# Kernel optimization log

Measured on AMD Instinct MI355X. Metric: run time of the kernel, lower is better.

The kernel has to match this reference:

```python
import jax, jax.numpy as jnp
import numpy as np

B, S, D, L = 2, 1024, 1024, 8
HQ, HK, DH = 16, 4, 64          # query heads, kv heads, head_dim = D // HQ
FF, V = 2816, 32000             # FFN hidden (2/3*4D rounded to 256), vocab
EPS = 1e-5
THETA = 500000.0


def setup_inputs() -> dict:
    key = jax.random.key(0)
    ks = jax.random.split(key, 12)
    s = 0.02
    n = lambda k, sh: jax.random.normal(k, sh, dtype=jnp.float32) * s
    return {
        "tokens": jax.random.randint(ks[0], (B, S), 0, V),
        "start_pos": 0,
        "tok_emb": n(ks[1], (V, D)),
        "wq": n(ks[2], (L, D, HQ * DH)),
        "wk": n(ks[3], (L, D, HK * DH)),
        "wv": n(ks[4], (L, D, HK * DH)),
        "wo": n(ks[5], (L, HQ * DH, D)),
        "w1": n(ks[6], (L, D, FF)),
        "w2": n(ks[7], (L, FF, D)),
        "w3": n(ks[8], (L, D, FF)),
        "attn_norm_w": jnp.ones((L, D), jnp.float32),
        "ffn_norm_w": jnp.ones((L, D), jnp.float32),
        "final_norm_w": jnp.ones((D,), jnp.float32),
        "out_w": n(ks[9], (D, V)),
    }


def _rope_cos_sin(start, seqlen):
    freqs = 1.0 / (THETA ** (jnp.arange(0, DH, 2, dtype=jnp.float32) / DH))  # [DH/2]
    t = jnp.arange(start, start + seqlen, dtype=jnp.float32)
    ang = jnp.outer(t, freqs)  # [S, DH/2]
    return jnp.cos(ang), jnp.sin(ang)


def _apply_rope(x, cos, sin):
    # x: [B,S,H,DH]; pairs (even, odd) rotated by complex freqs_cis, as in apply_rotary_emb
    xr = x.reshape(x.shape[:-1] + (DH // 2, 2))
    a, b = xr[..., 0], xr[..., 1]
    c = cos[None, :, None, :]
    s = sin[None, :, None, :]
    out = jnp.stack([a * c - b * s, a * s + b * c], axis=-1)
    return out.reshape(x.shape)


def _rmsnorm(x, w):
    return x * jax.lax.rsqrt(jnp.mean(x * x, axis=-1, keepdims=True) + EPS) * w


def reference(tokens, start_pos, tok_emb, wq, wk, wv, wo, w1, w2, w3,
              attn_norm_w, ffn_norm_w, final_norm_w, out_w):
    h = tok_emb[tokens]  # [B,S,D]
    cos, sin = _rope_cos_sin(start_pos, S)
    # strictly-upper-triangular -inf causal mask (seqlen > 1 branch)
    idx = jnp.arange(S)
    mask = jnp.where(idx[None, :] > idx[:, None], -jnp.inf, 0.0).astype(h.dtype)

    def block(h, p):
        wq_, wk_, wv_, wo_, w1_, w2_, w3_, anw, fnw = p
        x = _rmsnorm(h, anw)
        q = (x @ wq_).reshape(B, S, HQ, DH)
        k = (x @ wk_).reshape(B, S, HK, DH)
        v = (x @ wv_).reshape(B, S, HK, DH)
        q = _apply_rope(q, cos, sin)
        k = _apply_rope(k, cos, sin)
        # start_pos=0: cache slice [:, :seqlen] == freshly written k/v; GQA repeat_kv
        k = jnp.repeat(k, HQ // HK, axis=2)  # [B,S,HQ,DH]
        v = jnp.repeat(v, HQ // HK, axis=2)
        scores = jnp.einsum('bqhd,bkhd->bhqk', q, k) / (DH ** 0.5) + mask
        attn = jax.nn.softmax(scores.astype(jnp.float32), axis=-1).astype(q.dtype)
        o = jnp.einsum('bhqk,bkhd->bqhd', attn, v).reshape(B, S, HQ * DH)
        h = h + o @ wo_
        x2 = _rmsnorm(h, fnw)
        ff = (jax.nn.silu(x2 @ w1_) * (x2 @ w3_)) @ w2_
        return h + ff, None

    h, _ = jax.lax.scan(block, h, (wq, wk, wv, wo, w1, w2, w3, attn_norm_w, ffn_norm_w))
    return (_rmsnorm(h, final_norm_w) @ out_w).astype(jnp.float32)
```

## Files before the change

kernel.cpp:

```cpp
#include <hip/hip_runtime.h>
#include <hip/hip_bf16.h>

typedef __bf16 bf16;
typedef __bf16 bf16x8 __attribute__((ext_vector_type(8)));
typedef float f32x4 __attribute__((ext_vector_type(4)));

#define B_ 2
#define S_ 1024
#define D_ 1024
#define L_ 8
#define HQ_ 16
#define HK_ 4
#define DH_ 64
#define FF_ 2816
#define V_ 32000

#define LGKM0 { asm volatile("s_waitcnt lgkmcnt(0)" ::: "memory"); __builtin_amdgcn_sched_barrier(0); }

__global__ __launch_bounds__(256) void embed_k(const int* __restrict__ toks,
                                               const float* __restrict__ emb,
                                               float* __restrict__ h) {
  int row = blockIdx.x;
  int tok = toks[row];
  f32x4 v = *(const f32x4*)&emb[(size_t)tok * D_ + threadIdx.x * 4];
  *(f32x4*)&h[(size_t)row * D_ + threadIdx.x * 4] = v;
}

__global__ __launch_bounds__(256) void ropetab_k(float* __restrict__ tab) {
  int i = blockIdx.x * 256 + threadIdx.x;
  if (i >= S_ * 32) return;
  int d = i & 31, s = i >> 5;
  float f = expf(-(2.0f * d / 64.0f) * logf(500000.0f));
  float ang = (float)s * f;
  tab[i * 2]     = cosf(ang);
  tab[i * 2 + 1] = sinf(ang);
}

__global__ __launch_bounds__(256) void rmsnorm_k(const float* __restrict__ x,
                                                 const float* __restrict__ w,
                                                 bf16* __restrict__ out) {
  int row = blockIdx.x;
  const float* xr = x + (size_t)row * D_;
  int base = threadIdx.x * 4;
  f32x4 v = *(const f32x4*)&xr[base];
  float ss = v[0]*v[0] + v[1]*v[1] + v[2]*v[2] + v[3]*v[3];
  for (int m = 1; m < 64; m <<= 1) ss += __shfl_xor(ss, m, 64);
  __shared__ float partial[4];
  if ((threadIdx.x & 63) == 0) partial[threadIdx.x >> 6] = ss;
  __syncthreads();
  float tot = partial[0] + partial[1] + partial[2] + partial[3];
  float rr = rsqrtf(tot * (1.0f / D_) + 1e-5f);
  f32x4 wv = *(const f32x4*)&w[base];
  bf16* o = out + (size_t)row * D_ + base;
  o[0] = (bf16)(v[0] * rr * wv[0]);
  o[1] = (bf16)(v[1] * rr * wv[1]);
  o[2] = (bf16)(v[2] * rr * wv[2]);
  o[3] = (bf16)(v[3] * rr * wv[3]);
}

__global__ __launch_bounds__(256) void redrms_k(const float* __restrict__ p,
                                                float* __restrict__ h,
                                                const float* __restrict__ w,
                                                bf16* __restrict__ out) {
  int row = blockIdx.x;
  int base = threadIdx.x * 4;
  size_t ix = (size_t)row * D_ + base;
  f32x4 a = *(const f32x4*)&p[ix];
  f32x4 bb = *(const f32x4*)&p[ix + 2097152];
  f32x4 v = *(const f32x4*)&h[ix];
  v += a + bb;
  *(f32x4*)&h[ix] = v;
  float ss = v[0]*v[0] + v[1]*v[1] + v[2]*v[2] + v[3]*v[3];
  for (int m = 1; m < 64; m <<= 1) ss += __shfl_xor(ss, m, 64);
  __shared__ float partial[4];
  if ((threadIdx.x & 63) == 0) partial[threadIdx.x >> 6] = ss;
  __syncthreads();
  float tot = partial[0] + partial[1] + partial[2] + partial[3];
  float rr = rsqrtf(tot * (1.0f / D_) + 1e-5f);
  f32x4 wv = *(const f32x4*)&w[base];
  bf16* o = out + (size_t)row * D_ + base;
  o[0] = (bf16)(v[0] * rr * wv[0]);
  o[1] = (bf16)(v[1] * rr * wv[1]);
  o[2] = (bf16)(v[2] * rr * wv[2]);
  o[3] = (bf16)(v[3] * rr * wv[3]);
}

__global__ __launch_bounds__(256) void transpose_cvt(const float* __restrict__ src,
                                                     bf16* __restrict__ dst,
                                                     int K, int N,
                                                     long long srcStride, long long dstStride,
                                                     int rowMul, int rowAdd) {
  __shared__ float tile[32][33];
  int bx = blockIdx.x, by = blockIdx.y, z = blockIdx.z;
  src += (size_t)z * srcStride;
  dst += (size_t)z * dstStride;
  int tx = threadIdx.x & 31, ty = threadIdx.x >> 5;
#pragma unroll
  for (int i = 0; i < 4; ++i) {
    int r = ty + i * 8;
    tile[r][tx] = src[(size_t)(by * 32 + r) * N + bx * 32 + tx];
  }
  __syncthreads();
#pragma unroll
  for (int i = 0; i < 4; ++i) {
    int r = ty + i * 8;
    dst[(size_t)((bx * 32 + r) * rowMul + rowAdd) * K + by * 32 + tx] = (bf16)tile[tx][r];
  }
}

template <int EPI, int BM>
__global__ __launch_bounds__(256) void gemm_bt(const bf16* __restrict__ A,
                                               const bf16* __restrict__ BT,
                                               void* __restrict__ Cout,
                                               const float* __restrict__ R,
                                               int M, int N, int K,
                                               int lda, int ldb,
                                               int zKoff, long long partStride) {
  constexpr int MR = BM / 32;
  __shared__ bf16 As[BM * 64];
  __shared__ bf16 Bs[128 * 64];
  const int t = threadIdx.x;
  const int w = t >> 6, l = t & 63;
  const int l15 = l & 15, l4 = l >> 4;
  const int bm = blockIdx.x * BM, bn = blockIdx.y * 128;
  const int wr = w >> 1, wc = w & 1;
  const int z = blockIdx.z;

  const bf16* Az = A + (size_t)z * zKoff;
  const bf16* Bz = BT + (size_t)z * zKoff;
  float* Cz = (float*)Cout + (size_t)z * partStride;

  const int srow = t >> 3, scol = (t & 7) * 8;
  const bf16* ag = &Az[(size_t)(bm + srow) * lda + scol];
  const bf16* bg = &Bz[(size_t)(bn + srow) * ldb + scol];
  const int ldsbase = (t & 192) * 8;

  f32x4 acc[MR][4] = {};

  for (int k0 = 0; k0 < K; k0 += 64) {
#pragma unroll
    for (int i = 0; i < BM / 32; ++i)
      __builtin_amdgcn_global_load_lds(
          (const __attribute__((address_space(1))) void*)(ag + (size_t)(i * 32) * lda + k0),
          (__attribute__((address_space(3))) void*)&As[i * 2048 + ldsbase], 16, 0, 0);
#pragma unroll
    for (int i = 0; i < 4; ++i)
      __builtin_amdgcn_global_load_lds(
          (const __attribute__((address_space(1))) void*)(bg + (size_t)(i * 32) * ldb + k0),
          (__attribute__((address_space(3))) void*)&Bs[i * 2048 + ldsbase], 16, 0, 0);
    __syncthreads();
#pragma unroll
    for (int kc = 0; kc < 2; ++kc) {
      bf16x8 af[MR], bfr[4];
#pragma unroll
      for (int m = 0; m < MR; ++m)
        af[m] = *(const bf16x8*)&As[(wr * (BM / 2) + m * 16 + l15) * 64 + kc * 32 + l4 * 8];
#pragma unroll
      for (int n = 0; n < 4; ++n)
        bfr[n] = *(const bf16x8*)&Bs[(wc * 64 + n * 16 + l15) * 64 + kc * 32 + l4 * 8];
#pragma unroll
      for (int m = 0; m < MR; ++m)
#pragma unroll
        for (int n = 0; n < 4; ++n)
          acc[m][n] = __builtin_amdgcn_mfma_f32_16x16x32_bf16(af[m], bfr[n], acc[m][n], 0, 0, 0);
    }
    __syncthreads();
  }

#pragma unroll
  for (int m = 0; m < MR; ++m)
#pragma unroll
    for (int n = 0; n < 4; ++n)
#pragma unroll
      for (int r = 0; r < 4; ++r) {
        int row = bm + wr * (BM / 2) + m * 16 + l4 * 4 + r;
        int col = bn + wc * 64 + n * 16 + l15;
        size_t ix = (size_t)row * N + col;
        float v = acc[m][n][r];
        if (EPI == 0)      Cz[ix] = v;
        else               Cz[ix] = v + R[ix];
      }
}

template <int EPI>
__global__ __launch_bounds__(512, 2) void gemm256_bt(const bf16* __restrict__ A,
                                                     const bf16* __restrict__ BT,
                                                     void* __restrict__ Cout,
                                                     const float* __restrict__ R,
                                                     int N, int K) {
  extern __shared__ char smem[];
  const int t = threadIdx.x;
  const int wid = t >> 6, l = t & 63;
  const int l15 = l & 15, l4 = l >> 4;
  const int wr = wid >> 2, wc = wid & 3;
  const int rsw = (l4 ^ ((l15 >> 1) & 3)) * 16;
  const int csw = ((t & 3) ^ ((t >> 3) & 3)) * 8;

  int nwg = gridDim.x;
  int q = nwg >> 3, r = nwg & 7;
  int xcd = blockIdx.x & 7, jj = blockIdx.x >> 3;
  int L = (xcd < r ? xcd * (q + 1) : r * (q + 1) + (xcd - r) * q) + jj;
  const int bm = (L & 7) * 256, bn = (L >> 3) * 256;

  const int NT = K >> 6;

  auto stage = [&](const bf16* __restrict__ G, int rowbase, int cbase, int buf, int kc, int kt) {
#pragma unroll
    for (int i = 0; i < 2; ++i) {
      int j = i * 512 + t;
      const bf16* src = G + (size_t)(rowbase + (j >> 2)) * K + kt * 64 + kc * 32 + csw;
      __builtin_amdgcn_global_load_lds(
          (const __attribute__((address_space(1))) void*)src,
          (__attribute__((address_space(3))) void*)(smem + cbase + buf * 32768 + kc * 16384 +
                                                    i * 8192 + wid * 1024),
          16, 0, 0);
    }
  };
  auto ldA = [&](int buf, int kc, int m) -> bf16x8 {
    return *(const bf16x8*)(smem + buf * 32768 + kc * 16384 +
                            (wr * 128 + m * 16 + l15) * 64 + rsw);
  };
  auto ldB = [&](int buf, int kc, int n) -> bf16x8 {
    return *(const bf16x8*)(smem + 65536 + buf * 32768 + kc * 16384 +
                            (wc * 64 + n * 16 + l15) * 64 + rsw);
  };

  f32x4 acc[8][4] = {};
  bf16x8 af[4], bq[4];

  auto rd03 = [&](int buf, int kc) {
#pragma unroll
    for (int m = 0; m < 4; ++m) af[m] = ldA(buf, kc, m);
#pragma unroll
    for (int n = 0; n < 4; ++n) bq[n] = ldB(buf, kc, n);
  };
  auto rd47 = [&](int buf, int kc) {
#pragma unroll
    for (int m = 0; m < 4; ++m) af[m] = ldA(buf, kc, 4 + m);
  };
  auto mf_lo = [&]() {
    __builtin_amdgcn_s_setprio(1);
#pragma unroll
    for (int m = 0; m < 4; ++m)
#pragma unroll
      for (int n = 0; n < 4; ++n)
        acc[m][n] = __builtin_amdgcn_mfma_f32_16x16x32_bf16(af[m], bq[n], acc[m][n], 0, 0, 0);
    __builtin_amdgcn_s_setprio(0);
    __builtin_amdgcn_sched_barrier(0);
  };
  auto mf_hi = [&]() {
    __builtin_amdgcn_s_setprio(1);
#pragma unroll
    for (int m = 0; m < 4; ++m)
#pragma unroll
      for (int n = 0; n < 4; ++n)
        acc[4 + m][n] = __builtin_amdgcn_mfma_f32_16x16x32_bf16(af[m], bq[n], acc[4 + m][n], 0, 0, 0);
    __builtin_amdgcn_s_setprio(0);
    __builtin_amdgcn_sched_barrier(0);
  };
#define GBAR { __builtin_amdgcn_sched_barrier(0); __builtin_amdgcn_s_barrier(); }
#define VMW(n) { asm volatile("s_waitcnt vmcnt(" #n ")" ::: "memory"); __builtin_amdgcn_sched_barrier(0); }

  stage(A, bm, 0, 0, 0, 0);  stage(BT, bn, 65536, 0, 0, 0);
  stage(A, bm, 0, 0, 1, 0);  stage(BT, bn, 65536, 0, 1, 0);
  stage(A, bm, 0, 1, 0, 1);  stage(BT, bn, 65536, 1, 0, 1);
  VMW(8);
  __builtin_amdgcn_s_barrier();

  for (int kt = 0; kt < NT - 2; ++kt) {
    const int buf = kt & 1, nbuf = buf ^ 1;
    rd03(buf, 0);
    stage(A, bm, 0, nbuf, 1, kt + 1);
    GBAR; mf_lo(); GBAR;
    rd47(buf, 0);
    stage(BT, bn, 65536, nbuf, 1, kt + 1);
    GBAR; mf_hi(); VMW(8); __builtin_amdgcn_s_barrier();
    rd03(buf, 1);
    stage(A, bm, 0, buf, 0, kt + 2);
    stage(BT, bn, 65536, buf, 0, kt + 2);
    GBAR; mf_lo(); GBAR;
    rd47(buf, 1);
    GBAR; mf_hi(); VMW(8); __builtin_amdgcn_s_barrier();
  }
  {
    const int kt = NT - 2;
    const int buf = kt & 1, nbuf = buf ^ 1;
    rd03(buf, 0);
    stage(A, bm, 0, nbuf, 1, kt + 1);
    GBAR; mf_lo(); GBAR;
    rd47(buf, 0);
    stage(BT, bn, 65536, nbuf, 1, kt + 1);
    GBAR; mf_hi(); VMW(8); __builtin_amdgcn_s_barrier();
    rd03(buf, 1);
    GBAR; mf_lo(); GBAR;
    rd47(buf, 1);
    GBAR; mf_hi(); VMW(4); __builtin_amdgcn_s_barrier();
  }
  {
    const int buf = (NT - 1) & 1;
    rd03(buf, 0);
    GBAR; mf_lo(); GBAR;
    rd47(buf, 0);
    GBAR; mf_hi(); VMW(0); __builtin_amdgcn_s_barrier();
    rd03(buf, 1);
    GBAR; mf_lo(); GBAR;
    rd47(buf, 1);
    GBAR; mf_hi(); __builtin_amdgcn_s_barrier();
  }
#undef GBAR
#undef VMW

#pragma unroll
  for (int m = 0; m < 8; ++m)
#pragma unroll
    for (int n = 0; n < 4; ++n)
#pragma unroll
      for (int rr = 0; rr < 4; ++rr) {
        int row = bm + wr * 128 + m * 16 + l4 * 4 + rr;
        int col = bn + wc * 64 + n * 16 + l15;
        size_t ix = (size_t)row * N + col;
        float v = acc[m][n][rr];
        if (EPI == 0)      ((float*)Cout)[ix] = v;
        else if (EPI == 1) ((float*)Cout)[ix] = v + R[ix];
        else               ((bf16*)Cout)[ix] = (bf16)v;
      }
}

template <int EPI>
__global__ __launch_bounds__(512, 4) void gemm8_bt(const bf16* __restrict__ A,
                                                   const bf16* __restrict__ BT,
                                                   void* __restrict__ Cout,
                                                   const float* __restrict__ tab,
                                                   bf16* __restrict__ krout,
                                                   bf16* __restrict__ vtout,
                                                   int N, int K) {
  extern __shared__ char smem[];
  const int t = threadIdx.x;
  const int wid = t >> 6, l = t & 63;
  const int l15 = l & 15, l4 = l >> 4;
  const int wr = wid >> 1, wc = wid & 1;
  const int rsw = (l4 ^ ((l15 >> 1) & 3)) * 16;
  const int csw = ((t & 3) ^ ((t >> 3) & 3)) * 8;

  int nwg = gridDim.x;
  int q = nwg >> 3;
  int xcd = blockIdx.x & 7, jj = blockIdx.x >> 3;
  int L = xcd * q + jj;
  const int bm = (L & 15) * 128, bn = (L >> 4) * 128;

  const int NT = K >> 6;

  auto stage = [&](const bf16* __restrict__ G, int rowbase, int obase, int buf, int kc, int kt) {
    const bf16* src = G + (size_t)(rowbase + (t >> 2)) * K + kt * 64 + kc * 32 + csw;
    __builtin_amdgcn_global_load_lds(
        (const __attribute__((address_space(1))) void*)src,
        (__attribute__((address_space(3))) void*)(smem + obase + buf * 16384 + kc * 8192 +
                                                  wid * 1024),
        16, 0, 0);
  };
  auto ldA = [&](int buf, int kc, int m) -> bf16x8 {
    return *(const bf16x8*)(smem + buf * 16384 + kc * 8192 +
                            (wr * 32 + m * 16 + l15) * 64 + rsw);
  };
  auto ldB = [&](int buf, int kc, int n) -> bf16x8 {
    return *(const bf16x8*)(smem + 32768 + buf * 16384 + kc * 8192 +
                            (wc * 64 + n * 16 + l15) * 64 + rsw);
  };

  f32x4 acc[2][4] = {};
  bf16x8 af[2], bq[4];

  auto rdph = [&](int buf, int kc) {
#pragma unroll
    for (int m = 0; m < 2; ++m) af[m] = ldA(buf, kc, m);
#pragma unroll
    for (int n = 0; n < 4; ++n) bq[n] = ldB(buf, kc, n);
  };
  auto mf = [&]() {
    __builtin_amdgcn_s_setprio(1);
#pragma unroll
    for (int m = 0; m < 2; ++m)
#pragma unroll
      for (int n = 0; n < 4; ++n)
        acc[m][n] = __builtin_amdgcn_mfma_f32_16x16x32_bf16(af[m], bq[n], acc[m][n], 0, 0, 0);
    __builtin_amdgcn_s_setprio(0);
    __builtin_amdgcn_sched_barrier(0);
  };
#define SCB __builtin_amdgcn_sched_barrier(0)
#define VMW4 { asm volatile("s_waitcnt vmcnt(4)" ::: "memory"); SCB; }
#define VMW2 { asm volatile("s_waitcnt vmcnt(2)" ::: "memory"); SCB; }
#define VMW0 { asm volatile("s_waitcnt vmcnt(0)" ::: "memory"); SCB; }
#define SBAR { __builtin_amdgcn_s_barrier(); SCB; }

  stage(A, bm, 0, 0, 0, 0);  stage(BT, bn, 32768, 0, 0, 0);
  stage(A, bm, 0, 0, 1, 0);  stage(BT, bn, 32768, 0, 1, 0);
  stage(A, bm, 0, 1, 0, 1);  stage(BT, bn, 32768, 1, 0, 1);
  VMW4; __builtin_amdgcn_s_barrier();

  for (int kt = 0; kt < NT - 2; ++kt) {
    const int buf = kt & 1, nbuf = buf ^ 1;
    rdph(buf, 0);
    stage(A, bm, 0, nbuf, 1, kt + 1);
    stage(BT, bn, 32768, nbuf, 1, kt + 1);
    SCB; mf(); VMW4; SBAR;
    rdph(buf, 1);
    stage(A, bm, 0, buf, 0, kt + 2);
    stage(BT, bn, 32768, buf, 0, kt + 2);
    SCB; mf(); VMW4; SBAR;
  }
  {
    const int buf = (NT - 2) & 1, nbuf = buf ^ 1;
    rdph(buf, 0);
    stage(A, bm, 0, nbuf, 1, NT - 1);
    stage(BT, bn, 32768, nbuf, 1, NT - 1);
    SCB; mf(); VMW4; SBAR;
    rdph(buf, 1);
    SCB; mf(); VMW2; SBAR;
  }
  {
    const int buf = (NT - 1) & 1;
    rdph(buf, 0);
    SCB; mf(); VMW0; SBAR;
    rdph(buf, 1);
    SCB; mf();
  }
#undef SCB
#undef VMW4
#undef VMW2
#undef VMW0
#undef SBAR

  __builtin_amdgcn_s_barrier();

  if (EPI == 3) {
    bf16* wb = (bf16*)(smem + wid * 2304);
    bf16* G = (bf16*)Cout;
    const int Nc = N >> 1;
#pragma unroll
    for (int m = 0; m < 2; ++m) {
#pragma unroll
      for (int n = 0; n < 4; ++n)
#pragma unroll
        for (int rr = 0; rr < 4; ++rr) {
          float v = acc[m][n][rr];
          float part = __shfl_xor(v, 1, 64);
          if (!(l15 & 1)) {
            float s = v / (1.0f + __expf(-v));
            wb[(l4 * 4 + rr) * 40 + n * 8 + (l15 >> 1)] = (bf16)(s * part);
          }
        }
      LGKM0;
      int ROW = l >> 2, CB = l & 3;
      bf16x8 g = *(const bf16x8*)&wb[ROW * 40 + CB * 8];
      LGKM0;
      int row = bm + wr * 32 + m * 16 + ROW;
      int col = (bn >> 1) + wc * 32 + CB * 8;
      *(bf16x8*)&G[(size_t)row * Nc + col] = g;
    }
  } else {
    const int cb = bn >> 7;
    if (cb >= 10) {
      bf16* wbT = (bf16*)(smem + wid * 4352);
#pragma unroll
      for (int m = 0; m < 2; ++m)
#pragma unroll
        for (int n = 0; n < 4; ++n)
#pragma unroll
          for (int rr = 0; rr < 4; ++rr)
            wbT[(n * 16 + l15) * 34 + m * 16 + l4 * 4 + rr] = (bf16)acc[m][n][rr];
      LGKM0;
      bf16x8 v0 = *(const bf16x8*)&wbT[l * 34];
      bf16x8 v1 = *(const bf16x8*)&wbT[l * 34 + 8];
      bf16x8 v2 = *(const bf16x8*)&wbT[l * 34 + 16];
      bf16x8 v3 = *(const bf16x8*)&wbT[l * 34 + 24];
      LGKM0;
      int hh = ((bn - 1280) >> 6) + wc;
      int b = bm >> 10;
      int scol = (bm & 1023) + wr * 32;
      bf16* dst = &vtout[((size_t)((b * HK_ + hh) * 64 + l)) * S_ + scol];
      *(bf16x8*)&dst[0]  = v0;  *(bf16x8*)&dst[8]  = v1;
      *(bf16x8*)&dst[16] = v2;  *(bf16x8*)&dst[24] = v3;
    } else {
      bf16* wb = (bf16*)(smem + wid * 2304);
#pragma unroll
      for (int m = 0; m < 2; ++m) {
#pragma unroll
        for (int n = 0; n < 4; ++n)
#pragma unroll
          for (int rr = 0; rr < 4; ++rr)
            wb[(l4 * 4 + rr) * 72 + n * 16 + l15] = (bf16)acc[m][n][rr];
        LGKM0;
        int ROW = l >> 2, CB = l & 3;
        bf16x8 g0 = *(const bf16x8*)&wb[ROW * 72 + CB * 16];
        bf16x8 g1 = *(const bf16x8*)&wb[ROW * 72 + CB * 16 + 8];
        LGKM0;
        int row = bm + wr * 32 + m * 16 + ROW;
        if (cb < 8) {
          bf16* Cb = (bf16*)Cout;
          int col = bn + wc * 64 + CB * 16;
          *(bf16x8*)&Cb[(size_t)row * N + col] = g0;
          *(bf16x8*)&Cb[(size_t)row * N + col + 8] = g1;
        } else {
          int b = row >> 10, ss = row & 1023;
          int hh = ((bn - 1024) >> 6) + wc;
          int d0 = CB * 16;
          f32x4 t0 = *(const f32x4*)&tab[(ss * 32 + (d0 >> 1)) * 2];
          f32x4 t1 = *(const f32x4*)&tab[(ss * 32 + (d0 >> 1)) * 2 + 4];
          f32x4 t2 = *(const f32x4*)&tab[(ss * 32 + (d0 >> 1) + 4) * 2];
          f32x4 t3 = *(const f32x4*)&tab[(ss * 32 + (d0 >> 1) + 4) * 2 + 4];
          bf16x8 r0, r1;
#pragma unroll
          for (int j = 0; j < 4; ++j) {
            float a = (float)g0[2 * j], bv = (float)g0[2 * j + 1];
            float c  = (j < 2 ? t0 : t1)[(j & 1) * 2];
            float sn = (j < 2 ? t0 : t1)[(j & 1) * 2 + 1];
            r0[2 * j]     = (bf16)(a * c - bv * sn);
            r0[2 * j + 1] = (bf16)(a * sn + bv * c);
            float a2 = (float)g1[2 * j], bv2 = (float)g1[2 * j + 1];
            float c2  = (j < 2 ? t2 : t3)[(j & 1) * 2];
            float sn2 = (j < 2 ? t2 : t3)[(j & 1) * 2 + 1];
            r1[2 * j]     = (bf16)(a2 * c2 - bv2 * sn2);
            r1[2 * j + 1] = (bf16)(a2 * sn2 + bv2 * c2);
          }
          bf16* dst = &krout[((size_t)((b * HK_ + hh) * S_ + ss)) * 64 + d0];
          *(bf16x8*)&dst[0] = r0;
          *(bf16x8*)&dst[8] = r1;
        }
      }
    }
  }
}

__global__ __launch_bounds__(256) void attn_k(const bf16* __restrict__ qkv,
                                              const float* __restrict__ tab,
                                              const bf16* __restrict__ k_r,
                                              const bf16* __restrict__ vT,
                                              bf16* __restrict__ o) {
  __shared__ bf16 k_lds[128 * 64];
  __shared__ bf16 v_lds[64 * 128];
  __shared__ bf16 p_lds[4][16 * 136];
  int t = threadIdx.x, w = t >> 6, l = t & 63, l15 = l & 15, l4 = l >> 4;
  int bx = blockIdx.x;
  int qt = bx & 15;
  if (bx >= 256) qt = 15 - qt;
  int head = (bx >> 4) & 15, b = bx >> 8;
  int kvh = head >> 2;
  const bf16* kh = k_r + ((size_t)(b * HK_ + kvh)) * S_ * 64;
  const bf16* vh = vT + ((size_t)(b * HK_ + kvh)) * 64 * S_;
  int q0 = qt * 64 + w * 16;
  const int ntile = (qt + 2) >> 1;

  bf16x8 aq[2];
  {
    int s = q0 + l15;
#pragma unroll
    for (int kc = 0; kc < 2; ++kc) {
      bf16x8 raw = *(const bf16x8*)&qkv[(size_t)(b * S_ + s) * 1536 + head * 64 +
                                        kc * 32 + l4 * 8];
      int d0 = kc * 16 + l4 * 4;
      f32x4 tc0 = *(const f32x4*)&tab[(s * 32 + d0) * 2];
      f32x4 tc1 = *(const f32x4*)&tab[(s * 32 + d0) * 2 + 4];
      bf16x8 out;
#pragma unroll
      for (int j = 0; j < 4; ++j) {
        float a = (float)raw[2 * j], bb = (float)raw[2 * j + 1];
        float c  = (j < 2 ? tc0 : tc1)[(j & 1) * 2];
        float sn = (j < 2 ? tc0 : tc1)[(j & 1) * 2 + 1];
        out[2 * j]     = (bf16)((a * c - bb * sn) * 0.125f);
        out[2 * j + 1] = (bf16)((a * sn + bb * c) * 0.125f);
      }
      aq[kc] = out;
    }
  }

  f32x4 acc_o[4] = {};
  float m_run[4], l_run[4];
#pragma unroll
  for (int r = 0; r < 4; ++r) { m_run[r] = -1e30f; l_run[r] = 0.f; }

  bf16x8 gk[4], gv[4];
#pragma unroll
  for (int i = 0; i < 4; ++i) {
    int c = i * 256 + t;
    gk[i] = *(const bf16x8*)&kh[(size_t)(c >> 3) * 64 + (c & 7) * 8];
    gv[i] = *(const bf16x8*)&vh[(size_t)(c >> 4) * S_ + (c & 15) * 8];
  }

  for (int j = 0; j < ntile; ++j) {
#pragma unroll
    for (int i = 0; i < 4; ++i) {
      int c = i * 256 + t;
      int krow = c >> 3, kch = (c & 7) ^ (krow & 7);
      *(bf16x8*)&k_lds[krow * 64 + kch * 8] = gk[i];
      int vrow = c >> 4, vch = (c & 15) ^ (vrow & 15);
      *(bf16x8*)&v_lds[vrow * 128 + vch * 8] = gv[i];
    }
    __syncthreads();

    bf16x8 gkn[4], gvn[4];
    if (j + 1 < ntile) {
#pragma unroll
      for (int i = 0; i < 4; ++i) {
        int c = i * 256 + t;
        gkn[i] = *(const bf16x8*)&kh[(size_t)((j + 1) * 128 + (c >> 3)) * 64 + (c & 7) * 8];
        gvn[i] = *(const bf16x8*)&vh[(size_t)(c >> 4) * S_ + (j + 1) * 128 + (c & 15) * 8];
      }
    }

    f32x4 sc[8];
#pragma unroll
    for (int nt = 0; nt < 8; ++nt) {
      f32x4 a = {};
#pragma unroll
      for (int kc = 0; kc < 2; ++kc) {
        bf16x8 bk = *(const bf16x8*)&k_lds[(nt * 16 + l15) * 64 +
                                           (((kc * 4 + l4) ^ (l15 & 7)) * 8)];
        a = __builtin_amdgcn_mfma_f32_16x16x32_bf16(aq[kc], bk, a, 0, 0, 0);
      }
      sc[nt] = a;
    }

    bool lastt = (j == ntile - 1);
#pragma unroll
    for (int r = 0; r < 4; ++r) {
      float pmax = -1e30f;
#pragma unroll
      for (int nt = 0; nt < 8; ++nt) {
        float s = sc[nt][r];
        if (lastt) {
          int kj = j * 128 + nt * 16 + l15;
          int qi = q0 + l4 * 4 + r;
          if (kj > qi) s = -1e30f;
        }
        sc[nt][r] = s;
        pmax = fmaxf(pmax, s);
      }
      if (!__all(pmax <= m_run[r] + 8.0f)) {
        float mx = pmax;
        mx = fmaxf(mx, __shfl_xor(mx, 1, 64));
        mx = fmaxf(mx, __shfl_xor(mx, 2, 64));
        mx = fmaxf(mx, __shfl_xor(mx, 4, 64));
        mx = fmaxf(mx, __shfl_xor(mx, 8, 64));
        float mn = fmaxf(m_run[r], mx);
        float scale = __expf(m_run[r] - mn);
        m_run[r] = mn;
        l_run[r] *= scale;
#pragma unroll
        for (int nt = 0; nt < 4; ++nt) acc_o[nt][r] *= scale;
      }
      float rs = 0.f;
#pragma unroll
      for (int nt = 0; nt < 8; ++nt) {
        float p = __expf(sc[nt][r] - m_run[r]);
        sc[nt][r] = p;
        rs += p;
      }
      l_run[r] += rs;
    }

#pragma unroll
    for (int nt = 0; nt < 8; ++nt)
#pragma unroll
      for (int r = 0; r < 4; ++r)
        p_lds[w][(l4 * 4 + r) * 136 + nt * 16 + l15] = (bf16)sc[nt][r];
    LGKM0;

#pragma unroll
    for (int kc = 0; kc < 4; ++kc) {
      bf16x8 pf = *(const bf16x8*)&p_lds[w][l15 * 136 + kc * 32 + l4 * 8];
#pragma unroll
      for (int nt = 0; nt < 4; ++nt) {
        bf16x8 vf = *(const bf16x8*)&v_lds[(nt * 16 + l15) * 128 +
                                           (((kc * 4 + l4) ^ l15) * 8)];
        acc_o[nt] = __builtin_amdgcn_mfma_f32_16x16x32_bf16(pf, vf, acc_o[nt], 0, 0, 0);
      }
    }
    __syncthreads();

#pragma unroll
    for (int i = 0; i < 4; ++i) { gk[i] = gkn[i]; gv[i] = gvn[i]; }
  }

#pragma unroll
  for (int r = 0; r < 4; ++r) {
    float lr = l_run[r];
    lr += __shfl_xor(lr, 1, 64);
    lr += __shfl_xor(lr, 2, 64);
    lr += __shfl_xor(lr, 4, 64);
    lr += __shfl_xor(lr, 8, 64);
    l_run[r] = lr;
  }

#pragma unroll
  for (int nt = 0; nt < 4; ++nt)
#pragma unroll
    for (int r = 0; r < 4; ++r) {
      float ov = acc_o[nt][r] / l_run[r];
      int s = qt * 64 + w * 16 + l4 * 4 + r;
      o[((size_t)(b * S_ + s)) * D_ + head * 64 + nt * 16 + l15] = (bf16)ov;
    }
}

extern "C" void kernel_launch(void* const* d_in, const int* in_sizes, int n_in,
                              void* d_out, int out_size, void* d_ws, size_t ws_size,
                              hipStream_t stream) {
  const int* tokens  = (const int*)d_in[0];
  const float* tok_emb = (const float*)d_in[2];
  const float* wq = (const float*)d_in[3];
  const float* wk = (const float*)d_in[4];
  const float* wv = (const float*)d_in[5];
  const float* wo = (const float*)d_in[6];
  const float* w1 = (const float*)d_in[7];
  const float* w2 = (const float*)d_in[8];
  const float* w3 = (const float*)d_in[9];
  const float* anw = (const float*)d_in[10];
  const float* fnw = (const float*)d_in[11];
  const float* finw = (const float*)d_in[12];
  const float* outw = (const float*)d_in[13];

  (void)hipFuncSetAttribute((const void*)gemm256_bt<0>,
                            hipFuncAttributeMaxDynamicSharedMemorySize, 131072);
  (void)hipFuncSetAttribute((const void*)gemm8_bt<3>,
                            hipFuncAttributeMaxDynamicSharedMemorySize, 65536);
  (void)hipFuncSetAttribute((const void*)gemm8_bt<4>,
                            hipFuncAttributeMaxDynamicSharedMemorySize, 65536);

  auto al = [](size_t x) { return (x + 255) & ~(size_t)255; };
  const size_t WTB   = 11272192ull * 2;
  const size_t OUTWTB = (size_t)V_ * D_ * 2;
  const size_t HB   = (size_t)B_ * S_ * D_ * 4;
  const size_t XBB  = (size_t)B_ * S_ * D_ * 2;
  const size_t QKVB = (size_t)B_ * S_ * 1536 * 2;
  const size_t KRB  = (size_t)B_ * HK_ * S_ * 64 * 2;
  const size_t OB   = (size_t)B_ * S_ * D_ * 2;
  const size_t GATEB = (size_t)B_ * S_ * 2816 * 2;
  const size_t TABB = (size_t)S_ * 32 * 2 * 4;
  const size_t PARTB = (size_t)B_ * S_ * D_ * 4 * 2;

  size_t fixed = al(OUTWTB) + al(HB) + al(XBB) + al(QKVB) + al(KRB) + al(KRB) +
                 al(OB) + al(GATEB) + al(TABB) + al(PARTB);
  bool allup = ws_size >= fixed + 8 * al(WTB) + 4096;
  int nslots = allup ? 8 : 1;

  char* p = (char*)d_ws;
  bf16* wT    = (bf16*)p; p += (size_t)nslots * al(WTB);
  bf16* outwT = (bf16*)p; p += al(OUTWTB);
  float* h    = (float*)p; p += al(HB);
  bf16* xb    = (bf16*)p; p += al(XBB);
  bf16* qkv   = (bf16*)p; p += al(QKVB);
  bf16* k_r   = (bf16*)p; p += al(KRB);
  bf16* vTb   = (bf16*)p; p += al(KRB);
  bf16* ob    = (bf16*)p; p += al(OB);
  bf16* gate  = (bf16*)p; p += al(GATEB);
  float* tab  = (float*)p; p += al(TABB);
  float* part = (float*)p; p += al(PARTB);

  const size_t WTS = al(WTB) / 2;
  const size_t OFF_QKV = 0;
  const size_t OFF_WK  = 1024ull * 1024;
  const size_t OFF_WV  = 1280ull * 1024;
  const size_t OFF_WO  = 1572864ull;
  const size_t OFF_W13 = 2621440ull;
  const size_t OFF_W2  = 8388608ull;

  auto tr = [&](const float* src, size_t srcStride, bf16* dst, size_t dstStride,
                int Kd, int Nd, int layers, int rowMul, int rowAdd) {
    transpose_cvt<<<dim3(Nd / 32, Kd / 32, layers), 256, 0, stream>>>(
        src, dst, Kd, Nd, (long long)srcStride, (long long)dstStride, rowMul, rowAdd);
  };

  ropetab_k<<<128, 256, 0, stream>>>(tab);
  embed_k<<<B_ * S_, 256, 0, stream>>>(tokens, tok_emb, h);
  tr(outw, 0, outwT, 0, 1024, 32000, 1, 1, 0);

  if (allup) {
    tr(wq, 1024 * 1024, wT + OFF_QKV, WTS, 1024, 1024, 8, 1, 0);
    tr(wk, 1024 * 256,  wT + OFF_WK,  WTS, 1024, 256, 8, 1, 0);
    tr(wv, 1024 * 256,  wT + OFF_WV,  WTS, 1024, 256, 8, 1, 0);
    tr(wo, 1024 * 1024, wT + OFF_WO,  WTS, 1024, 1024, 8, 1, 0);
    tr(w1, 1024 * 2816, wT + OFF_W13, WTS, 1024, 2816, 8, 2, 0);
    tr(w3, 1024 * 2816, wT + OFF_W13, WTS, 1024, 2816, 8, 2, 1);
    tr(w2, 2816 * 1024, wT + OFF_W2,  WTS, 2816, 1024, 8, 1, 0);
  }

  rmsnorm_k<<<B_ * S_, 256, 0, stream>>>(h, anw, xb);

  for (int l = 0; l < L_; ++l) {
    bf16* wtl = wT + (allup ? (size_t)l * WTS : 0);
    if (!allup) {
      tr(wq + (size_t)l * 1024 * 1024, 0, wtl + OFF_QKV, 0, 1024, 1024, 1, 1, 0);
      tr(wk + (size_t)l * 1024 * 256,  0, wtl + OFF_WK,  0, 1024, 256, 1, 1, 0);
      tr(wv + (size_t)l * 1024 * 256,  0, wtl + OFF_WV,  0, 1024, 256, 1, 1, 0);
      tr(wo + (size_t)l * 1024 * 1024, 0, wtl + OFF_WO,  0, 1024, 1024, 1, 1, 0);
      tr(w1 + (size_t)l * 1024 * 2816, 0, wtl + OFF_W13, 0, 1024, 2816, 1, 2, 0);
      tr(w3 + (size_t)l * 1024 * 2816, 0, wtl + OFF_W13, 0, 1024, 2816, 1, 2, 1);
      tr(w2 + (size_t)l * 2816 * 1024, 0, wtl + OFF_W2,  0, 2816, 1024, 1, 1, 0);
    }

    gemm8_bt<4><<<192, 512, 65536, stream>>>(xb, wtl + OFF_QKV, qkv, tab, k_r, vTb,
                                             1536, 1024);
    attn_k<<<B_ * HQ_ * (S_ / 64), 256, 0, stream>>>(qkv, tab, k_r, vTb, ob);
    gemm_bt<1, 32><<<dim3(64, 8, 1), 256, 0, stream>>>(ob, wtl + OFF_WO, h, h,
                                                       2048, 1024, 1024, 1024, 1024, 0, 0);
    rmsnorm_k<<<B_ * S_, 256, 0, stream>>>(h, fnw + l * D_, xb);
    gemm8_bt<3><<<704, 512, 65536, stream>>>(xb, wtl + OFF_W13, gate, nullptr, nullptr,
                                             nullptr, 5632, 1024);
    gemm_bt<0, 64><<<dim3(32, 8, 2), 256, 0, stream>>>(gate, wtl + OFF_W2, part, nullptr,
                                                       2048, 1024, 1408, 2816, 2816,
                                                       1408, 2097152ll);
    redrms_k<<<B_ * S_, 256, 0, stream>>>(part, h,
                                          (l < L_ - 1) ? (anw + (l + 1) * D_) : finw, xb);
  }

  gemm256_bt<0><<<1000, 512, 131072, stream>>>(xb, outwT, d_out, nullptr, 32000, 1024);
}
```

Measured before the change: 1.452 ms.

## Vectorize weight transpose-convert with 64x64 tiles and fuse embedding with RMSNorm

The weight transpose/bf16 conversion kernel now moves 64x64 tiles using 16-byte float4 loads and 8-wide bf16 stores instead of scalar 32x32 accesses. This aims to cut the memory-bound cost of converting all layer weights and the output projection on every call. Separately, the token embedding gather is fused with the first attention RMSNorm so the hidden row is not re-read by a separate kernel. The strided LDS reads in the transpose may incur some bank conflicts.

```diff
diff --git a/kernel.cpp b/kernel.cpp
--- a/kernel.cpp
+++ b/kernel.cpp
@@ -17,13 +17,29 @@
 
 #define LGKM0 { asm volatile("s_waitcnt lgkmcnt(0)" ::: "memory"); __builtin_amdgcn_sched_barrier(0); }
 
-__global__ __launch_bounds__(256) void embed_k(const int* __restrict__ toks,
-                                               const float* __restrict__ emb,
-                                               float* __restrict__ h) {
+__global__ __launch_bounds__(256) void embedrms_k(const int* __restrict__ toks,
+                                                  const float* __restrict__ emb,
+                                                  const float* __restrict__ w,
+                                                  float* __restrict__ h,
+                                                  bf16* __restrict__ out) {
   int row = blockIdx.x;
   int tok = toks[row];
-  f32x4 v = *(const f32x4*)&emb[(size_t)tok * D_ + threadIdx.x * 4];
-  *(f32x4*)&h[(size_t)row * D_ + threadIdx.x * 4] = v;
+  int base = threadIdx.x * 4;
+  f32x4 v = *(const f32x4*)&emb[(size_t)tok * D_ + base];
+  *(f32x4*)&h[(size_t)row * D_ + base] = v;
+  float ss = v[0]*v[0] + v[1]*v[1] + v[2]*v[2] + v[3]*v[3];
+  for (int m = 1; m < 64; m <<= 1) ss += __shfl_xor(ss, m, 64);
+  __shared__ float partial[4];
+  if ((threadIdx.x & 63) == 0) partial[threadIdx.x >> 6] = ss;
+  __syncthreads();
+  float tot = partial[0] + partial[1] + partial[2] + partial[3];
+  float rr = rsqrtf(tot * (1.0f / D_) + 1e-5f);
+  f32x4 wv = *(const f32x4*)&w[base];
+  bf16* o = out + (size_t)row * D_ + base;
+  o[0] = (bf16)(v[0] * rr * wv[0]);
+  o[1] = (bf16)(v[1] * rr * wv[1]);
+  o[2] = (bf16)(v[2] * rr * wv[2]);
+  o[3] = (bf16)(v[3] * rr * wv[3]);
 }
 
 __global__ __launch_bounds__(256) void ropetab_k(float* __restrict__ tab) {
@@ -90,21 +106,27 @@
                                                      int K, int N,
                                                      long long srcStride, long long dstStride,
                                                      int rowMul, int rowAdd) {
-  __shared__ float tile[32][33];
+  __shared__ float tile[64][68];
   int bx = blockIdx.x, by = blockIdx.y, z = blockIdx.z;
   src += (size_t)z * srcStride;
   dst += (size_t)z * dstStride;
-  int tx = threadIdx.x & 31, ty = threadIdx.x >> 5;
-#pragma unroll
-  for (int i = 0; i < 4; ++i) {
-    int r = ty + i * 8;
-    tile[r][tx] = src[(size_t)(by * 32 + r) * N + bx * 32 + tx];
+  int t = threadIdx.x;
+#pragma unroll
+  for (int it = 0; it < 4; ++it) {
+    int idx = it * 256 + t;
+    int r = idx >> 4, c4 = (idx & 15) * 4;
+    f32x4 v = *(const f32x4*)&src[(size_t)(by * 64 + r) * N + bx * 64 + c4];
+    *(f32x4*)&tile[r][c4] = v;
   }
   __syncthreads();
 #pragma unroll
-  for (int i = 0; i < 4; ++i) {
-    int r = ty + i * 8;
-    dst[(size_t)((bx * 32 + r) * rowMul + rowAdd) * K + by * 32 + tx] = (bf16)tile[tx][r];
+  for (int it = 0; it < 2; ++it) {
+    int idx = it * 256 + t;
+    int n = idx >> 3, k8 = (idx & 7) * 8;
+    bf16x8 o;
+#pragma unroll
+    for (int j = 0; j < 8; ++j) o[j] = (bf16)tile[k8 + j][n];
+    *(bf16x8*)&dst[(size_t)((bx * 64 + n) * rowMul + rowAdd) * K + by * 64 + k8] = o;
   }
 }
 
@@ -765,12 +787,12 @@
 
   auto tr = [&](const float* src, size_t srcStride, bf16* dst, size_t dstStride,
                 int Kd, int Nd, int layers, int rowMul, int rowAdd) {
-    transpose_cvt<<<dim3(Nd / 32, Kd / 32, layers), 256, 0, stream>>>(
+    transpose_cvt<<<dim3(Nd / 64, Kd / 64, layers), 256, 0, stream>>>(
         src, dst, Kd, Nd, (long long)srcStride, (long long)dstStride, rowMul, rowAdd);
   };
 
   ropetab_k<<<128, 256, 0, stream>>>(tab);
-  embed_k<<<B_ * S_, 256, 0, stream>>>(tokens, tok_emb, h);
+  embedrms_k<<<B_ * S_, 256, 0, stream>>>(tokens, tok_emb, anw, h, xb);
   tr(outw, 0, outwT, 0, 1024, 32000, 1, 1, 0);
 
   if (allup) {
@@ -782,8 +804,6 @@
     tr(w3, 1024 * 2816, wT + OFF_W13, WTS, 1024, 2816, 8, 2, 1);
     tr(w2, 2816 * 1024, wT + OFF_W2,  WTS, 2816, 1024, 8, 1, 0);
   }
-
-  rmsnorm_k<<<B_ * S_, 256, 0, stream>>>(h, anw, xb);
 
   for (int l = 0; l < L_; ++l) {
     bf16* wtl = wT + (allup ? (size_t)l * WTS : 0);
```

Result: no change. 1.438 ms (-1.0%).
